# Kernel tuning notes

Measured on AMD Instinct MI355X. Metric: run time of the kernel, lower is better.

The kernel has to match this reference:

```python
import jax, jax.numpy as jnp
import numpy as np

ORDER, IN_DIM, OUT_DIM, SEQ_LEN = 4096, 8, 1, 4096


def setup_inputs() -> dict:
    key = jax.random.key(0)
    ks = jax.random.split(key, 7)
    # reset_parameter uses uniform(-0.7, 0.7); A/C/L rescaled ~1/sqrt(order) for
    # numerical stability of the 4096-step linear recurrence (same math, stable values).
    sA = 0.9 * (3.0 / ORDER) ** 0.5
    sC = 0.7 / ORDER ** 0.5
    weight_a = jax.random.uniform(ks[0], (ORDER, ORDER), minval=-sA, maxval=sA, dtype=jnp.float32)
    weight_b = jax.random.uniform(ks[1], (ORDER, IN_DIM), minval=-0.7, maxval=0.7, dtype=jnp.float32)
    weight_c = jax.random.uniform(ks[2], (OUT_DIM, ORDER), minval=-sC, maxval=sC, dtype=jnp.float32)
    weight_d = jax.random.uniform(ks[3], (OUT_DIM, IN_DIM), minval=-0.7, maxval=0.7, dtype=jnp.float32)
    weight_l = jax.random.uniform(ks[4], (ORDER, 1), minval=-sC, maxval=sC, dtype=jnp.float32)
    u = jax.random.normal(ks[5], (IN_DIM, SEQ_LEN), dtype=jnp.float32)
    y_obs = jax.random.normal(ks[6], (1, SEQ_LEN), dtype=jnp.float32)
    return {"u": u, "y_obs": y_obs, "weight_a": weight_a, "weight_b": weight_b,
            "weight_c": weight_c, "weight_d": weight_d, "weight_l": weight_l}


def reference(u, y_obs, weight_a, weight_b, weight_c, weight_d, weight_l):
    # Observer (Luenberger) state-space recursion, inp_dim > 1 branch:
    #   y_t  = C h_t + D u_t
    #   h_{t+1} = A h_t + B u_t + L * (y_obs_t - y_t)
    # output = tanh(concat(y_t)) * 3, shape [out_dim, seq_len]
    order = weight_a.shape[0]
    h0 = jnp.ones((order, 1), dtype=u.dtype)  # nn.init.constant_(hidden, 1)

    def step(h, inp):
        u_t, yobs_t = inp  # u_t: [in_dim, 1], yobs_t: scalar
        y_t = weight_c @ h + weight_d @ u_t          # [out_dim, 1]
        h_next = weight_a @ h + weight_b @ u_t + weight_l * (yobs_t - y_t)
        return h_next, y_t

    u_seq = u.T[:, :, None]          # [seq_len, in_dim, 1]
    _, ys = jax.lax.scan(step, h0, (u_seq, y_obs[0]))
    y_hat = ys[:, :, 0].T            # [out_dim, seq_len]
    return jnp.tanh(y_hat) * 3
```

## Files before the change

### kernel.cpp

```cpp
#include <hip/hip_runtime.h>
#include <math.h>


constexpr int NDIM  = 4096;
constexpr int NC    = 10;
constexpr int SLAB  = 16 * 4096;
constexpr int JT    = 56;
constexpr int VAPPS = 28;
constexpr int KC    = NDIM / 32;
constexpr int TILES = NDIM / 16;

typedef float    f32x4  __attribute__((ext_vector_type(4)));
typedef _Float16 h16x8  __attribute__((ext_vector_type(8)));
typedef _Float16 f16;

__global__ __launch_bounds__(256) void k_build_a(
        const float* __restrict__ A, const float* __restrict__ C,
        const float* __restrict__ L, h16x8* __restrict__ AhSw) {
    __shared__ float lds[64][65];
    const int R0 = (blockIdx.x & 63) * 64;
    const int C0 = (blockIdx.x >> 6) * 64;
    const int tid = threadIdx.x;
    #pragma unroll
    for (int it = 0; it < 16; ++it) {
        const int r = it * 4 + (tid >> 6);
        const int c = tid & 63;
        lds[r][c] = A[(size_t)(R0 + r) * NDIM + C0 + c]
                  - L[R0 + r] * C[C0 + c];
    }
    __syncthreads();
    #pragma unroll
    for (int half = 0; half < 2; ++half) {
        const int o = half * 256 + tid;
        const int r = o >> 3;
        const int g = o & 7;
        union { h16x8 v; f16 h[8]; } pk;
        #pragma unroll
        for (int j = 0; j < 8; ++j) pk.h[j] = (f16)lds[r][g * 8 + j];
        const int tile = (R0 >> 4) + (r >> 4);
        const int kc   = (C0 >> 5) + (g >> 2);
        const int lane = (r & 15) | ((g & 3) << 4);
        AhSw[((size_t)tile * KC + kc) * 64 + lane] = pk.v;
    }
}

__global__ __launch_bounds__(256) void k_build_w0(
        const float* __restrict__ Bm, const float* __restrict__ Dm,
        const float* __restrict__ L,
        float* __restrict__ Wf, f16* __restrict__ Wh) {
    int k = blockIdx.x * blockDim.x + threadIdx.x;
    float Lk = L[k];
    float col[16];
    #pragma unroll
    for (int c = 0; c < 8; ++c) col[c] = Bm[k * 8 + c] - Lk * Dm[c];
    col[8] = Lk; col[9] = 1.0f;
    #pragma unroll
    for (int c = 10; c < 16; ++c) col[c] = 0.0f;
    #pragma unroll
    for (int c = 0; c < 16; ++c) {
        Wf[c * NDIM + k] = col[c];
        Wh[c * NDIM + k] = (f16)col[c];
    }
}

__global__ __launch_bounds__(256) void k_stepVR(
        const h16x8* __restrict__ AhSw, const f16* __restrict__ WhIn,
        float* __restrict__ WfOut, f16* __restrict__ WhOut,
        const float* __restrict__ Cvec,
        const float* __restrict__ RpartIn, float* __restrict__ RpartOut,
        float* __restrict__ gfSlot, const int r) {
    const int tid = threadIdx.x;

    if (blockIdx.x < 128) {
        __shared__ f32x4 red[4][64];
        const int lane = tid & 63, wave = tid >> 6;
        const int mr   = lane & 15, q = lane >> 4;
        const int tp   = blockIdx.x;
        const int tile = tp * 2 + (wave >> 1);
        const int kh   = wave & 1;
        const int k0   = kh * 2048;
        const bool liveB = (mr < NC);
        const h16x8* a8 = AhSw + ((size_t)tile * KC + kh * 64) * 64 + lane;
        const h16x8* b8 = (const h16x8*)WhIn + (((size_t)mr * NDIM + k0) >> 3) + q;

        f32x4 acc0 = {0,0,0,0}, acc1 = {0,0,0,0};
        for (int it = 0; it < 8; ++it) {
            h16x8 ra[8], rb[8];
            #pragma unroll
            for (int s = 0; s < 8; ++s) rb[s] = (h16x8){0,0,0,0,0,0,0,0};
            #pragma unroll
            for (int s = 0; s < 8; ++s) {
                const int c = it * 8 + s;
                ra[s] = a8[(size_t)c * 64];
            }
            if (liveB) {
                #pragma unroll
                for (int s = 0; s < 8; ++s) {
                    const int c = it * 8 + s;
                    rb[s] = b8[c * 4];
                }
            }
            #pragma unroll
            for (int s = 0; s < 8; ++s) {
                if (s & 1) acc1 = __builtin_amdgcn_mfma_f32_16x16x32_f16(ra[s], rb[s], acc1, 0, 0, 0);
                else       acc0 = __builtin_amdgcn_mfma_f32_16x16x32_f16(ra[s], rb[s], acc0, 0, 0, 0);
            }
        }
        red[wave][lane] = acc0 + acc1;
        __syncthreads();
        if (tid < 128) {
            const int half = tid >> 6;
            const int l    = tid & 63;
            f32x4 v = red[half * 2][l] + red[half * 2 + 1][l];
            const int col = l & 15;
            if (col < NC) {
                const int row0 = (tp * 2 + half) * 16;
                const int rb0  = row0 + ((l >> 4) << 2);
                #pragma unroll
                for (int i = 0; i < 4; ++i) {
                    WfOut[col * NDIM + rb0 + i] = v[i];
                    WhOut[col * NDIM + rb0 + i] = (f16)v[i];
                }
            }
        }
    } else {
        __shared__ float rp[4096];
        __shared__ float g8[8][33];
        __shared__ float gs[32];
        const int t = blockIdx.x - 128;

        if (r == 0) {
            if (tid < 32) gs[tid] = Cvec[t * 32 + tid];
        } else {
            #pragma unroll
            for (int i = 0; i < 16; ++i) {
                const int idx = tid + i * 256;
                rp[idx] = RpartIn[(size_t)(idx >> 5) * NDIM + t * 32 + (idx & 31)];
            }
            __syncthreads();
            {
                const int c = tid & 31, g = tid >> 5;
                float s = 0.0f;
                #pragma unroll
                for (int j = 0; j < 16; ++j) s += rp[(g * 16 + j) * 32 + c];
                g8[g][c] = s;
            }
            __syncthreads();
            if (tid < 32) {
                float s = 0.0f;
                #pragma unroll
                for (int g = 0; g < 8; ++g) s += g8[g][tid];
                gs[tid] = s;
            }
        }
        __syncthreads();
        if (tid < 32) gfSlot[t * 32 + tid] = gs[tid];

        if (r < VAPPS - 1) {
            float gl[32];
            #pragma unroll
            for (int j = 0; j < 32; ++j) gl[j] = gs[j];
            #pragma unroll
            for (int cc = 0; cc < 2; ++cc) {
                const int ch = tid * 2 + cc;
                float acc[8] = {};
                #pragma unroll
                for (int tt = 0; tt < 2; ++tt) {
                    const h16x8* fr = AhSw + (size_t)(t * 2 + tt) * (KC * 64)
                                    + (size_t)ch * 16;
                    #pragma unroll
                    for (int mrr = 0; mrr < 16; ++mrr) {
                        union { h16x8 v; f16 h[8]; } ua;
                        ua.v = fr[mrr];
                        const float gm = gl[tt * 16 + mrr];
                        #pragma unroll
                        for (int j = 0; j < 8; ++j) acc[j] += gm * (float)ua.h[j];
                    }
                }
                float4* op = (float4*)(RpartOut + (size_t)t * NDIM + 8 * ch);
                op[0] = make_float4(acc[0], acc[1], acc[2], acc[3]);
                op[1] = make_float4(acc[4], acc[5], acc[6], acc[7]);
            }
        }
    }
}

__global__ __launch_bounds__(256) void k_fbatch(
        const float* __restrict__ Wall, const float* __restrict__ C,
        const float* __restrict__ gf, float* __restrict__ F) {
    const int m = blockIdx.x;
    const float* W;
    const float* vec;
    if (m <= VAPPS) { W = Wall + (size_t)m * SLAB;     vec = C; }
    else            { W = Wall + (size_t)VAPPS * SLAB; vec = gf + (size_t)(m - VAPPS) * NDIM; }
    const int tid = threadIdx.x, lane = tid & 63, wave = tid >> 6;
    float acc[NC] = {};
    for (int k = tid; k < NDIM; k += 256) {
        float ck = vec[k];
        #pragma unroll
        for (int c = 0; c < NC; ++c) acc[c] += ck * W[c * NDIM + k];
    }
    __shared__ float red[4][NC];
    #pragma unroll
    for (int c = 0; c < NC; ++c) {
        float s = acc[c];
        #pragma unroll
        for (int off = 32; off > 0; off >>= 1) s += __shfl_down(s, off);
        if (lane == 0) red[wave][c] = s;
    }
    __syncthreads();
    if (tid < NC) F[m * NC + tid] = red[0][tid] + red[1][tid] + red[2][tid] + red[3][tid];
}

__global__ __launch_bounds__(256) void k_conv(
        const float* __restrict__ F, const float* __restrict__ u,
        const float* __restrict__ yobs, const float* __restrict__ Dm,
        float* __restrict__ out) {
    __shared__ float Fl[JT * NC];
    __shared__ float zw[(JT + 256) * 9];
    const int tid = threadIdx.x;
    const int t0  = blockIdx.x * 256;
    for (int idx = tid; idx < JT * NC; idx += 256) Fl[idx] = F[idx];
    for (int idx = tid; idx < (JT + 256) * 9; idx += 256) {
        int k = idx / 9, c = idx - k * 9;
        int s = t0 - JT + k;
        float v = 0.0f;
        if (s >= 0 && s < NDIM) v = (c < 8) ? u[c * NDIM + s] : yobs[s];
        zw[idx] = v;
    }
    __syncthreads();
    const int t = t0 + tid;
    float y = (t < JT) ? Fl[t * NC + 9] : 0.0f;
    #pragma unroll
    for (int c = 0; c < 8; ++c) y += Dm[c] * u[c * NDIM + t];
    for (int j = 0; j < JT; ++j) {
        const float* fj = Fl + j * NC;
        const float* zz = zw + (tid + JT - 1 - j) * 9;
        float p = 0.0f;
        #pragma unroll
        for (int c = 0; c < 9; ++c) p += fj[c] * zz[c];
        y += p;
    }
    out[t] = 3.0f * tanhf(y);
}

extern "C" void kernel_launch(void* const* d_in, const int* in_sizes, int n_in,
                              void* d_out, int out_size, void* d_ws, size_t ws_size,
                              hipStream_t stream) {
    const float* u    = (const float*)d_in[0];
    const float* yobs = (const float*)d_in[1];
    const float* A    = (const float*)d_in[2];
    const float* Bm   = (const float*)d_in[3];
    const float* C    = (const float*)d_in[4];
    const float* Dm   = (const float*)d_in[5];
    const float* L    = (const float*)d_in[6];
    float* out = (float*)d_out;

    char* ws = (char*)d_ws;
    h16x8* AhSw  = (h16x8*)ws;
    float* Wf    = (float*)(ws + 33554432ull);
    f16*   Wh    = (f16*)(ws + 41156608ull);
    float* gf    = (float*)(ws + 44957696ull);
    float* Rpart = (float*)(ws + 45416448ull);
    float* F     = (float*)(ws + 49610752ull);

    constexpr size_t RPN = (size_t)128 * NDIM;

    k_build_a<<<dim3(64 * 64), dim3(256), 0, stream>>>(A, C, L, AhSw);
    k_build_w0<<<dim3(16), dim3(256), 0, stream>>>(Bm, Dm, L, Wf, Wh);

    for (int r = 0; r < VAPPS; ++r) {
        const size_t in   = (size_t)r * SLAB;
        const size_t out_ = (size_t)(r + 1) * SLAB;
        const float* rin  = Rpart + ((r + 1) & 1) * RPN;
        float*       rout = Rpart + (r & 1) * RPN;
        k_stepVR<<<dim3(256), dim3(256), 0, stream>>>(
            AhSw, Wh + in, Wf + out_, Wh + out_,
            C, rin, rout, gf + (size_t)r * NDIM, r);
    }

    k_fbatch<<<dim3(JT), dim3(256), 0, stream>>>(Wf, C, gf, F);
    k_conv<<<dim3(16), dim3(256), 0, stream>>>(F, u, yobs, Dm, out);
}
```

Measured before the change: 462.3 us.

## Fuse transposed A-vector product into MFMA step blocks, reusing loaded A fragments

The step kernel no longer splits its blocks into MFMA tiles and a separate set of blocks that reload A for the g·A product. Each of the 256 blocks now owns one 16-row tile, splits K across four waves, and computes the row-vector partials from the A fragments already held in registers, reducing them with cross-lane shuffles. The goal is to read A only once per step and balance work across all blocks. In exchange it adds shuffle-heavy ALU work inside the MFMA loop and doubles the size of the partial-sum buffer, which makes the reduction at the start of the next step larger.

```diff
diff --git a/kernel.cpp b/kernel.cpp
--- a/kernel.cpp
+++ b/kernel.cpp
@@ -63,123 +63,120 @@
     }
 }
 
-__global__ __launch_bounds__(256) void k_stepVR(
+__global__ __launch_bounds__(256) void k_step(
         const h16x8* __restrict__ AhSw, const f16* __restrict__ WhIn,
         float* __restrict__ WfOut, f16* __restrict__ WhOut,
         const float* __restrict__ Cvec,
         const float* __restrict__ RpartIn, float* __restrict__ RpartOut,
         float* __restrict__ gfSlot, const int r) {
-    const int tid = threadIdx.x;
-
-    if (blockIdx.x < 128) {
-        __shared__ f32x4 red[4][64];
-        const int lane = tid & 63, wave = tid >> 6;
-        const int mr   = lane & 15, q = lane >> 4;
-        const int tp   = blockIdx.x;
-        const int tile = tp * 2 + (wave >> 1);
-        const int kh   = wave & 1;
-        const int k0   = kh * 2048;
-        const bool liveB = (mr < NC);
-        const h16x8* a8 = AhSw + ((size_t)tile * KC + kh * 64) * 64 + lane;
-        const h16x8* b8 = (const h16x8*)WhIn + (((size_t)mr * NDIM + k0) >> 3) + q;
-
-        f32x4 acc0 = {0,0,0,0}, acc1 = {0,0,0,0};
-        for (int it = 0; it < 8; ++it) {
-            h16x8 ra[8], rb[8];
-            #pragma unroll
-            for (int s = 0; s < 8; ++s) rb[s] = (h16x8){0,0,0,0,0,0,0,0};
+    __shared__ f32x4 red[4][64];
+    __shared__ float rp[256][17];
+    __shared__ float g16[16][17];
+    __shared__ float gs[16];
+    const int tid  = threadIdx.x;
+    const int lane = tid & 63, wave = tid >> 6;
+    const int mr   = lane & 15, q = lane >> 4;
+    const int tile = blockIdx.x;
+    const int row0 = tile * 16;
+    const int k0   = wave * 1024;
+
+    if (r == 0) {
+        if (tid < 16) gs[tid] = Cvec[row0 + tid];
+    } else {
+        const float* src = RpartIn + (size_t)tid * NDIM + row0;
+        #pragma unroll
+        for (int j = 0; j < 16; j += 4) {
+            float4 v = *(const float4*)(src + j);
+            rp[tid][j] = v.x; rp[tid][j+1] = v.y;
+            rp[tid][j+2] = v.z; rp[tid][j+3] = v.w;
+        }
+        __syncthreads();
+        {
+            const int c = tid & 15, g = tid >> 4;
+            float s = 0.0f;
+            #pragma unroll
+            for (int j = 0; j < 16; ++j) s += rp[g * 16 + j][c];
+            g16[g][c] = s;
+        }
+        __syncthreads();
+        if (tid < 16) {
+            float s = 0.0f;
+            #pragma unroll
+            for (int g = 0; g < 16; ++g) s += g16[g][tid];
+            gs[tid] = s;
+        }
+    }
+    __syncthreads();
+    if (tid < 16) gfSlot[row0 + tid] = gs[tid];
+    const float gmr = gs[mr];
+    const bool doR = (r < VAPPS - 1);
+
+    const bool liveB = (mr < NC);
+    const h16x8* a8 = AhSw + ((size_t)tile * KC + wave * 32) * 64 + lane;
+    const h16x8* b8 = (const h16x8*)WhIn + (((size_t)mr * NDIM + k0) >> 3) + q;
+    float* rpo = RpartOut + (size_t)tile * NDIM;
+
+    f32x4 acc0 = {0,0,0,0}, acc1 = {0,0,0,0};
+    for (int it = 0; it < 4; ++it) {
+        h16x8 ra[8], rb[8];
+        #pragma unroll
+        for (int s = 0; s < 8; ++s) rb[s] = (h16x8){0,0,0,0,0,0,0,0};
+        #pragma unroll
+        for (int s = 0; s < 8; ++s) {
+            const int c = it * 8 + s;
+            ra[s] = a8[(size_t)c * 64];
+        }
+        if (liveB) {
             #pragma unroll
             for (int s = 0; s < 8; ++s) {
                 const int c = it * 8 + s;
-                ra[s] = a8[(size_t)c * 64];
+                rb[s] = b8[c * 4];
             }
-            if (liveB) {
+        }
+        #pragma unroll
+        for (int s = 0; s < 8; ++s) {
+            if (s & 1) acc1 = __builtin_amdgcn_mfma_f32_16x16x32_f16(ra[s], rb[s], acc1, 0, 0, 0);
+            else       acc0 = __builtin_amdgcn_mfma_f32_16x16x32_f16(ra[s], rb[s], acc0, 0, 0, 0);
+        }
+        if (doR) {
+            #pragma unroll
+            for (int s = 0; s < 8; ++s) {
+                union { h16x8 v; f16 h[8]; } ua;
+                ua.v = ra[s];
+                float p[8];
                 #pragma unroll
-                for (int s = 0; s < 8; ++s) {
-                    const int c = it * 8 + s;
-                    rb[s] = b8[c * 4];
+                for (int j = 0; j < 8; ++j) p[j] = gmr * (float)ua.h[j];
+                #pragma unroll
+                for (int off = 1; off < 16; off <<= 1) {
+                    #pragma unroll
+                    for (int j = 0; j < 8; ++j)
+                        p[j] += __shfl_xor(p[j], off, 16);
+                }
+                const float s01 = (mr & 1) ? p[1] : p[0];
+                const float s23 = (mr & 1) ? p[3] : p[2];
+                const float s45 = (mr & 1) ? p[5] : p[4];
+                const float s67 = (mr & 1) ? p[7] : p[6];
+                const float s03 = (mr & 2) ? s23 : s01;
+                const float s47 = (mr & 2) ? s67 : s45;
+                const float sel = (mr & 4) ? s47 : s03;
+                if (mr < 8) {
+                    const int kcG = wave * 32 + it * 8 + s;
+                    rpo[kcG * 32 + q * 8 + mr] = sel;
                 }
             }
-            #pragma unroll
-            for (int s = 0; s < 8; ++s) {
-                if (s & 1) acc1 = __builtin_amdgcn_mfma_f32_16x16x32_f16(ra[s], rb[s], acc1, 0, 0, 0);
-                else       acc0 = __builtin_amdgcn_mfma_f32_16x16x32_f16(ra[s], rb[s], acc0, 0, 0, 0);
-            }
-        }
-        red[wave][lane] = acc0 + acc1;
-        __syncthreads();
-        if (tid < 128) {
-            const int half = tid >> 6;
-            const int l    = tid & 63;
-            f32x4 v = red[half * 2][l] + red[half * 2 + 1][l];
-            const int col = l & 15;
-            if (col < NC) {
-                const int row0 = (tp * 2 + half) * 16;
-                const int rb0  = row0 + ((l >> 4) << 2);
-                #pragma unroll
-                for (int i = 0; i < 4; ++i) {
-                    WfOut[col * NDIM + rb0 + i] = v[i];
-                    WhOut[col * NDIM + rb0 + i] = (f16)v[i];
-                }
-            }
-        }
-    } else {
-        __shared__ float rp[4096];
-        __shared__ float g8[8][33];
-        __shared__ float gs[32];
-        const int t = blockIdx.x - 128;
-
-        if (r == 0) {
-            if (tid < 32) gs[tid] = Cvec[t * 32 + tid];
-        } else {
-            #pragma unroll
-            for (int i = 0; i < 16; ++i) {
-                const int idx = tid + i * 256;
-                rp[idx] = RpartIn[(size_t)(idx >> 5) * NDIM + t * 32 + (idx & 31)];
-            }
-            __syncthreads();
-            {
-                const int c = tid & 31, g = tid >> 5;
-                float s = 0.0f;
-                #pragma unroll
-                for (int j = 0; j < 16; ++j) s += rp[(g * 16 + j) * 32 + c];
-                g8[g][c] = s;
-            }
-            __syncthreads();
-            if (tid < 32) {
-                float s = 0.0f;
-                #pragma unroll
-                for (int g = 0; g < 8; ++g) s += g8[g][tid];
-                gs[tid] = s;
-            }
-        }
-        __syncthreads();
-        if (tid < 32) gfSlot[t * 32 + tid] = gs[tid];
-
-        if (r < VAPPS - 1) {
-            float gl[32];
-            #pragma unroll
-            for (int j = 0; j < 32; ++j) gl[j] = gs[j];
-            #pragma unroll
-            for (int cc = 0; cc < 2; ++cc) {
-                const int ch = tid * 2 + cc;
-                float acc[8] = {};
-                #pragma unroll
-                for (int tt = 0; tt < 2; ++tt) {
-                    const h16x8* fr = AhSw + (size_t)(t * 2 + tt) * (KC * 64)
-                                    + (size_t)ch * 16;
-                    #pragma unroll
-                    for (int mrr = 0; mrr < 16; ++mrr) {
-                        union { h16x8 v; f16 h[8]; } ua;
-                        ua.v = fr[mrr];
-                        const float gm = gl[tt * 16 + mrr];
-                        #pragma unroll
-                        for (int j = 0; j < 8; ++j) acc[j] += gm * (float)ua.h[j];
-                    }
-                }
-                float4* op = (float4*)(RpartOut + (size_t)t * NDIM + 8 * ch);
-                op[0] = make_float4(acc[0], acc[1], acc[2], acc[3]);
-                op[1] = make_float4(acc[4], acc[5], acc[6], acc[7]);
+        }
+    }
+    red[wave][lane] = acc0 + acc1;
+    __syncthreads();
+    if (tid < 64) {
+        f32x4 v = red[0][tid] + red[1][tid] + red[2][tid] + red[3][tid];
+        const int col = tid & 15;
+        if (col < NC) {
+            const int rb0 = row0 + ((tid >> 4) << 2);
+            #pragma unroll
+            for (int i = 0; i < 4; ++i) {
+                WfOut[col * NDIM + rb0 + i] = v[i];
+                WhOut[col * NDIM + rb0 + i] = (f16)v[i];
             }
         }
     }
@@ -262,9 +259,9 @@
     f16*   Wh    = (f16*)(ws + 41156608ull);
     float* gf    = (float*)(ws + 44957696ull);
     float* Rpart = (float*)(ws + 45416448ull);
-    float* F     = (float*)(ws + 49610752ull);
-
-    constexpr size_t RPN = (size_t)128 * NDIM;
+    float* F     = (float*)(ws + 53805056ull);
+
+    constexpr size_t RPN = (size_t)256 * NDIM;
 
     k_build_a<<<dim3(64 * 64), dim3(256), 0, stream>>>(A, C, L, AhSw);
     k_build_w0<<<dim3(16), dim3(256), 0, stream>>>(Bm, Dm, L, Wf, Wh);
@@ -274,7 +271,7 @@
         const size_t out_ = (size_t)(r + 1) * SLAB;
         const float* rin  = Rpart + ((r + 1) & 1) * RPN;
         float*       rout = Rpart + (r & 1) * RPN;
-        k_stepVR<<<dim3(256), dim3(256), 0, stream>>>(
+        k_step<<<dim3(256), dim3(256), 0, stream>>>(
             AhSw, Wh + in, Wf + out_, Wh + out_,
             C, rin, rout, gf + (size_t)r * NDIM, r);
     }
```

New measurement: 696.2 us. 1.51x slower.

## Fuse per-step kernel launches into one persistent cooperative kernel with grid barriers

Applied to the files above, without the earlier changes.

Replaces the 28 separate k_stepVR launches with a single cooperative persistent kernel. Blocks step through all iterations and synchronise through atomic counters in global memory, using cache-bypassing loads and stores. MFMA blocks now stage the full f16 B slab into LDS each step, replacing the per-wave global reads. This is meant to remove launch overhead and inter-kernel gaps. In exchange it adds spin-barrier latency, requires all 256 blocks to be co-resident, and loads each slab redundantly into every block's LDS.

```diff
diff --git a/kernel.cpp b/kernel.cpp
--- a/kernel.cpp
+++ b/kernel.cpp
@@ -9,6 +9,7 @@
 constexpr int VAPPS = 28;
 constexpr int KC    = NDIM / 32;
 constexpr int TILES = NDIM / 16;
+constexpr size_t RPN = (size_t)128 * NDIM;
 
 typedef float    f32x4  __attribute__((ext_vector_type(4)));
 typedef _Float16 h16x8  __attribute__((ext_vector_type(8)));
@@ -47,8 +48,10 @@
 __global__ __launch_bounds__(256) void k_build_w0(
         const float* __restrict__ Bm, const float* __restrict__ Dm,
         const float* __restrict__ L,
-        float* __restrict__ Wf, f16* __restrict__ Wh) {
+        float* __restrict__ Wf, f16* __restrict__ Wh,
+        unsigned int* __restrict__ flags) {
     int k = blockIdx.x * blockDim.x + threadIdx.x;
+    if (k < 64) flags[k] = 0u;
     float Lk = L[k];
     float col[16];
     #pragma unroll
@@ -63,124 +66,201 @@
     }
 }
 
-__global__ __launch_bounds__(256) void k_stepVR(
-        const h16x8* __restrict__ AhSw, const f16* __restrict__ WhIn,
-        float* __restrict__ WfOut, f16* __restrict__ WhOut,
-        const float* __restrict__ Cvec,
-        const float* __restrict__ RpartIn, float* __restrict__ RpartOut,
-        float* __restrict__ gfSlot, const int r) {
-    const int tid = threadIdx.x;
-
-    if (blockIdx.x < 128) {
-        __shared__ f32x4 red[4][64];
-        const int lane = tid & 63, wave = tid >> 6;
-        const int mr   = lane & 15, q = lane >> 4;
-        const int tp   = blockIdx.x;
+__global__ __launch_bounds__(256, 1) void k_persist(
+        const h16x8* __restrict__ AhSw, f16* __restrict__ WhB,
+        float* __restrict__ Wf, const float* __restrict__ Cvec,
+        float* __restrict__ gf, float* __restrict__ Rpart,
+        unsigned int* __restrict__ flags) {
+    __shared__ f16   Bst[10][4104];
+    __shared__ f32x4 red[4][64];
+    __shared__ float rp[128][36];
+    __shared__ float g8v[8][33];
+    __shared__ float gs[32];
+    const int tid  = threadIdx.x;
+    const int bid  = blockIdx.x;
+    const int lane = tid & 63, wave = tid >> 6;
+    const int mr   = lane & 15, q = lane >> 4;
+
+    if (bid < 128) {
+        const int tp = bid;
         const int tile = tp * 2 + (wave >> 1);
         const int kh   = wave & 1;
-        const int k0   = kh * 2048;
         const bool liveB = (mr < NC);
-        const h16x8* a8 = AhSw + ((size_t)tile * KC + kh * 64) * 64 + lane;
-        const h16x8* b8 = (const h16x8*)WhIn + (((size_t)mr * NDIM + k0) >> 3) + q;
-
-        f32x4 acc0 = {0,0,0,0}, acc1 = {0,0,0,0};
-        for (int it = 0; it < 8; ++it) {
-            h16x8 ra[8], rb[8];
-            #pragma unroll
-            for (int s = 0; s < 8; ++s) rb[s] = (h16x8){0,0,0,0,0,0,0,0};
-            #pragma unroll
-            for (int s = 0; s < 8; ++s) {
-                const int c = it * 8 + s;
-                ra[s] = a8[(size_t)c * 64];
-            }
-            if (liveB) {
+        const h16x8* a8 = AhSw + ((size_t)tile * KC + (size_t)kh * 64) * 64 + lane;
+        const f16* bl = &Bst[0][0] + (size_t)mr * 4104 + kh * 2048 + q * 8;
+
+        for (int r = 0; r < VAPPS; ++r) {
+            {
+                const f16* p = WhB + (size_t)r * SLAB + (size_t)tid * 160;
+                f32x4 b0,b1,b2,b3,b4,b5,b6,b7,b8,b9,b10,b11,b12,b13,b14,b15,b16,b17,b18,b19;
+                asm volatile(
+                    "global_load_dwordx4 %0, %20, off sc0 sc1\n\t"
+                    "global_load_dwordx4 %1, %20, off offset:16 sc0 sc1\n\t"
+                    "global_load_dwordx4 %2, %20, off offset:32 sc0 sc1\n\t"
+                    "global_load_dwordx4 %3, %20, off offset:48 sc0 sc1\n\t"
+                    "global_load_dwordx4 %4, %20, off offset:64 sc0 sc1\n\t"
+                    "global_load_dwordx4 %5, %20, off offset:80 sc0 sc1\n\t"
+                    "global_load_dwordx4 %6, %20, off offset:96 sc0 sc1\n\t"
+                    "global_load_dwordx4 %7, %20, off offset:112 sc0 sc1\n\t"
+                    "global_load_dwordx4 %8, %20, off offset:128 sc0 sc1\n\t"
+                    "global_load_dwordx4 %9, %20, off offset:144 sc0 sc1\n\t"
+                    "global_load_dwordx4 %10, %20, off offset:160 sc0 sc1\n\t"
+                    "global_load_dwordx4 %11, %20, off offset:176 sc0 sc1\n\t"
+                    "global_load_dwordx4 %12, %20, off offset:192 sc0 sc1\n\t"
+                    "global_load_dwordx4 %13, %20, off offset:208 sc0 sc1\n\t"
+                    "global_load_dwordx4 %14, %20, off offset:224 sc0 sc1\n\t"
+                    "global_load_dwordx4 %15, %20, off offset:240 sc0 sc1\n\t"
+                    "global_load_dwordx4 %16, %20, off offset:256 sc0 sc1\n\t"
+                    "global_load_dwordx4 %17, %20, off offset:272 sc0 sc1\n\t"
+                    "global_load_dwordx4 %18, %20, off offset:288 sc0 sc1\n\t"
+                    "global_load_dwordx4 %19, %20, off offset:304 sc0 sc1\n\t"
+                    "s_waitcnt vmcnt(0)"
+                    : "=&v"(b0),"=&v"(b1),"=&v"(b2),"=&v"(b3),"=&v"(b4),
+                      "=&v"(b5),"=&v"(b6),"=&v"(b7),"=&v"(b8),"=&v"(b9),
+                      "=&v"(b10),"=&v"(b11),"=&v"(b12),"=&v"(b13),"=&v"(b14),
+                      "=&v"(b15),"=&v"(b16),"=&v"(b17),"=&v"(b18),"=&v"(b19)
+                    : "v"(p) : "memory");
+                f32x4 bb[20] = {b0,b1,b2,b3,b4,b5,b6,b7,b8,b9,b10,b11,
+                                b12,b13,b14,b15,b16,b17,b18,b19};
+                const int u0 = tid * 20;
+                #pragma unroll
+                for (int i = 0; i < 20; ++i) {
+                    const int u = u0 + i;
+                    union { f32x4 f; h16x8 h; } cv; cv.f = bb[i];
+                    *(h16x8*)&Bst[u >> 9][(u & 511) * 8] = cv.h;
+                }
+            }
+            __syncthreads();
+
+            f32x4 acc0 = {0,0,0,0}, acc1 = {0,0,0,0};
+            for (int it = 0; it < 8; ++it) {
+                h16x8 ra[8], rb[8];
+                #pragma unroll
+                for (int s = 0; s < 8; ++s) rb[s] = (h16x8){0,0,0,0,0,0,0,0};
+                #pragma unroll
+                for (int s = 0; s < 8; ++s) ra[s] = a8[(size_t)(it * 8 + s) * 64];
+                if (liveB) {
+                    #pragma unroll
+                    for (int s = 0; s < 8; ++s)
+                        rb[s] = *(const h16x8*)(bl + (it * 8 + s) * 32);
+                }
                 #pragma unroll
                 for (int s = 0; s < 8; ++s) {
-                    const int c = it * 8 + s;
-                    rb[s] = b8[c * 4];
-                }
-            }
-            #pragma unroll
-            for (int s = 0; s < 8; ++s) {
-                if (s & 1) acc1 = __builtin_amdgcn_mfma_f32_16x16x32_f16(ra[s], rb[s], acc1, 0, 0, 0);
-                else       acc0 = __builtin_amdgcn_mfma_f32_16x16x32_f16(ra[s], rb[s], acc0, 0, 0, 0);
-            }
-        }
-        red[wave][lane] = acc0 + acc1;
-        __syncthreads();
-        if (tid < 128) {
-            const int half = tid >> 6;
-            const int l    = tid & 63;
-            f32x4 v = red[half * 2][l] + red[half * 2 + 1][l];
-            const int col = l & 15;
-            if (col < NC) {
-                const int row0 = (tp * 2 + half) * 16;
-                const int rb0  = row0 + ((l >> 4) << 2);
-                #pragma unroll
-                for (int i = 0; i < 4; ++i) {
-                    WfOut[col * NDIM + rb0 + i] = v[i];
-                    WhOut[col * NDIM + rb0 + i] = (f16)v[i];
-                }
-            }
+                    if (s & 1) acc1 = __builtin_amdgcn_mfma_f32_16x16x32_f16(ra[s], rb[s], acc1, 0, 0, 0);
+                    else       acc0 = __builtin_amdgcn_mfma_f32_16x16x32_f16(ra[s], rb[s], acc0, 0, 0, 0);
+                }
+            }
+            red[wave][lane] = acc0 + acc1;
+            __syncthreads();
+            if (tid < 128) {
+                const int half = tid >> 6, l = tid & 63;
+                f32x4 v = red[half * 2][l] + red[half * 2 + 1][l];
+                const int col = l & 15;
+                if (col < NC) {
+                    const int rb0 = (tp * 2 + half) * 16 + ((l >> 4) << 2);
+                    float* wf = Wf + (size_t)(r + 1) * SLAB + (size_t)col * NDIM + rb0;
+                    #pragma unroll
+                    for (int i = 0; i < 4; ++i)
+                        __builtin_nontemporal_store(v[i], wf + i);
+                    union { f16 h[4]; int2 u2; } pk;
+                    #pragma unroll
+                    for (int i = 0; i < 4; ++i) pk.h[i] = (f16)v[i];
+                    f16* wh = WhB + (size_t)(r + 1) * SLAB + (size_t)col * NDIM + rb0;
+                    asm volatile("global_store_dwordx2 %0, %1, off sc0 sc1"
+                                 :: "v"(wh), "v"(pk.u2) : "memory");
+                }
+            }
+            asm volatile("s_waitcnt vmcnt(0)" ::: "memory");
+            __syncthreads();
+            if (tid == 0) {
+                __hip_atomic_fetch_add(&flags[r], 1u, __ATOMIC_RELAXED, __HIP_MEMORY_SCOPE_AGENT);
+                while (__hip_atomic_load(&flags[r], __ATOMIC_RELAXED, __HIP_MEMORY_SCOPE_AGENT) < 256u)
+                    __builtin_amdgcn_s_sleep(2);
+            }
+            __syncthreads();
         }
     } else {
-        __shared__ float rp[4096];
-        __shared__ float g8[8][33];
-        __shared__ float gs[32];
-        const int t = blockIdx.x - 128;
-
-        if (r == 0) {
-            if (tid < 32) gs[tid] = Cvec[t * 32 + tid];
-        } else {
-            #pragma unroll
-            for (int i = 0; i < 16; ++i) {
-                const int idx = tid + i * 256;
-                rp[idx] = RpartIn[(size_t)(idx >> 5) * NDIM + t * 32 + (idx & 31)];
-            }
-            __syncthreads();
-            {
-                const int c = tid & 31, g = tid >> 5;
-                float s = 0.0f;
-                #pragma unroll
-                for (int j = 0; j < 16; ++j) s += rp[(g * 16 + j) * 32 + c];
-                g8[g][c] = s;
-            }
-            __syncthreads();
-            if (tid < 32) {
-                float s = 0.0f;
-                #pragma unroll
-                for (int g = 0; g < 8; ++g) s += g8[g][tid];
-                gs[tid] = s;
-            }
-        }
-        __syncthreads();
-        if (tid < 32) gfSlot[t * 32 + tid] = gs[tid];
-
-        if (r < VAPPS - 1) {
-            float gl[32];
-            #pragma unroll
-            for (int j = 0; j < 32; ++j) gl[j] = gs[j];
-            #pragma unroll
-            for (int cc = 0; cc < 2; ++cc) {
-                const int ch = tid * 2 + cc;
-                float acc[8] = {};
-                #pragma unroll
-                for (int tt = 0; tt < 2; ++tt) {
-                    const h16x8* fr = AhSw + (size_t)(t * 2 + tt) * (KC * 64)
-                                    + (size_t)ch * 16;
-                    #pragma unroll
-                    for (int mrr = 0; mrr < 16; ++mrr) {
-                        union { h16x8 v; f16 h[8]; } ua;
-                        ua.v = fr[mrr];
-                        const float gm = gl[tt * 16 + mrr];
+        const int t = bid - 128;
+        for (int r = 0; r < VAPPS; ++r) {
+            if (r == 0) {
+                if (tid < 32) gs[tid] = Cvec[t * 32 + tid];
+                __syncthreads();
+            } else {
+                const float* RpIn = Rpart + (size_t)((r + 1) & 1) * RPN;
+                const int p = tid >> 1, c0 = (tid & 1) * 16;
+                const float* q4 = RpIn + (size_t)p * NDIM + t * 32 + c0;
+                f32x4 v0, v1, v2, v3;
+                asm volatile(
+                    "global_load_dwordx4 %0, %4, off sc0 sc1\n\t"
+                    "global_load_dwordx4 %1, %4, off offset:16 sc0 sc1\n\t"
+                    "global_load_dwordx4 %2, %4, off offset:32 sc0 sc1\n\t"
+                    "global_load_dwordx4 %3, %4, off offset:48 sc0 sc1\n\t"
+                    "s_waitcnt vmcnt(0)"
+                    : "=&v"(v0), "=&v"(v1), "=&v"(v2), "=&v"(v3)
+                    : "v"(q4) : "memory");
+                *(f32x4*)&rp[p][c0]      = v0;
+                *(f32x4*)&rp[p][c0 + 4]  = v1;
+                *(f32x4*)&rp[p][c0 + 8]  = v2;
+                *(f32x4*)&rp[p][c0 + 12] = v3;
+                __syncthreads();
+                {
+                    const int c = tid & 31, g = tid >> 5;
+                    float s = 0.0f;
+                    #pragma unroll
+                    for (int j = 0; j < 16; ++j) s += rp[g * 16 + j][c];
+                    g8v[g][c] = s;
+                }
+                __syncthreads();
+                if (tid < 32) {
+                    float s = 0.0f;
+                    #pragma unroll
+                    for (int g = 0; g < 8; ++g) s += g8v[g][tid];
+                    gs[tid] = s;
+                }
+                __syncthreads();
+            }
+            if (tid < 32)
+                __builtin_nontemporal_store(gs[tid], gf + (size_t)r * NDIM + t * 32 + tid);
+
+            if (r < VAPPS - 1) {
+                float gl[32];
+                #pragma unroll
+                for (int j = 0; j < 32; ++j) gl[j] = gs[j];
+                float* RpOut = Rpart + (size_t)(r & 1) * RPN + (size_t)t * NDIM;
+                #pragma unroll
+                for (int cc = 0; cc < 2; ++cc) {
+                    const int ch = tid * 2 + cc;
+                    float acc[8] = {};
+                    #pragma unroll
+                    for (int tt = 0; tt < 2; ++tt) {
+                        const h16x8* fr = AhSw + (size_t)(t * 2 + tt) * (KC * 64)
+                                        + (size_t)ch * 16;
                         #pragma unroll
-                        for (int j = 0; j < 8; ++j) acc[j] += gm * (float)ua.h[j];
+                        for (int mrr = 0; mrr < 16; ++mrr) {
+                            union { h16x8 v; f16 h[8]; } ua;
+                            ua.v = fr[mrr];
+                            const float gm = gl[tt * 16 + mrr];
+                            #pragma unroll
+                            for (int j = 0; j < 8; ++j) acc[j] += gm * (float)ua.h[j];
+                        }
                     }
-                }
-                float4* op = (float4*)(RpartOut + (size_t)t * NDIM + 8 * ch);
-                op[0] = make_float4(acc[0], acc[1], acc[2], acc[3]);
-                op[1] = make_float4(acc[4], acc[5], acc[6], acc[7]);
-            }
+                    f32x4 o0 = {acc[0], acc[1], acc[2], acc[3]};
+                    f32x4 o1 = {acc[4], acc[5], acc[6], acc[7]};
+                    float* op = RpOut + 8 * ch;
+                    asm volatile(
+                        "global_store_dwordx4 %0, %2, off sc0 sc1\n\t"
+                        "global_store_dwordx4 %1, %3, off sc0 sc1"
+                        :: "v"(op), "v"(op + 4), "v"(o0), "v"(o1) : "memory");
+                }
+            }
+            asm volatile("s_waitcnt vmcnt(0)" ::: "memory");
+            __syncthreads();
+            if (tid == 0) {
+                __hip_atomic_fetch_add(&flags[r], 1u, __ATOMIC_RELAXED, __HIP_MEMORY_SCOPE_AGENT);
+                while (__hip_atomic_load(&flags[r], __ATOMIC_RELAXED, __HIP_MEMORY_SCOPE_AGENT) < 256u)
+                    __builtin_amdgcn_s_sleep(2);
+            }
+            __syncthreads();
         }
     }
 }
@@ -257,26 +337,22 @@
     float* out = (float*)d_out;
 
     char* ws = (char*)d_ws;
-    h16x8* AhSw  = (h16x8*)ws;
-    float* Wf    = (float*)(ws + 33554432ull);
-    f16*   Wh    = (f16*)(ws + 41156608ull);
-    float* gf    = (float*)(ws + 44957696ull);
-    float* Rpart = (float*)(ws + 45416448ull);
-    float* F     = (float*)(ws + 49610752ull);
-
-    constexpr size_t RPN = (size_t)128 * NDIM;
+    h16x8*        AhSw  = (h16x8*)ws;
+    float*        Wf    = (float*)(ws + 33554432ull);
+    f16*          Wh    = (f16*)(ws + 41156608ull);
+    float*        gf    = (float*)(ws + 44957696ull);
+    float*        Rpart = (float*)(ws + 45416448ull);
+    float*        F     = (float*)(ws + 49610752ull);
+    unsigned int* flags = (unsigned int*)(ws + 49614848ull);
 
     k_build_a<<<dim3(64 * 64), dim3(256), 0, stream>>>(A, C, L, AhSw);
-    k_build_w0<<<dim3(16), dim3(256), 0, stream>>>(Bm, Dm, L, Wf, Wh);
-
-    for (int r = 0; r < VAPPS; ++r) {
-        const size_t in   = (size_t)r * SLAB;
-        const size_t out_ = (size_t)(r + 1) * SLAB;
-        const float* rin  = Rpart + ((r + 1) & 1) * RPN;
-        float*       rout = Rpart + (r & 1) * RPN;
-        k_stepVR<<<dim3(256), dim3(256), 0, stream>>>(
-            AhSw, Wh + in, Wf + out_, Wh + out_,
-            C, rin, rout, gf + (size_t)r * NDIM, r);
+    k_build_w0<<<dim3(16), dim3(256), 0, stream>>>(Bm, Dm, L, Wf, Wh, flags);
+
+    {
+        void* args[] = { (void*)&AhSw, (void*)&Wh, (void*)&Wf, (void*)&C,
+                         (void*)&gf, (void*)&Rpart, (void*)&flags };
+        (void)hipLaunchCooperativeKernel((const void*)k_persist, dim3(256), dim3(256),
+                                         args, 0u, stream);
     }
 
     k_fbatch<<<dim3(JT), dim3(256), 0, stream>>>(Wf, C, gf, F);
```

New measurement: 773.4 us. 1.67x slower.

## Quantize A-LC to 12-bit per-row scaled ints split into 8+4 bit planes

Applied to the files above, without the earlier changes.

Adds a per-row absmax pass and a quantization kernel that stores the fp16 A−LC matrix as a signed 8-bit high plane plus a 4-bit nibble plane with per-row scales. The repeated step kernels read these 12-bit values, dequantize them to fp16 in registers for MFMA and for the VR reduction, and apply the row scale on output. The goal is to cut the bytes of A read in each of the 28 step launches. In exchange it adds an extra setup kernel, ALU work for unpacking, and a 12-bit precision loss on A.

```diff
diff --git a/kernel.cpp b/kernel.cpp
--- a/kernel.cpp
+++ b/kernel.cpp
@@ -16,7 +16,8 @@
 
 __global__ __launch_bounds__(256) void k_build_a(
         const float* __restrict__ A, const float* __restrict__ C,
-        const float* __restrict__ L, h16x8* __restrict__ AhSw) {
+        const float* __restrict__ L, h16x8* __restrict__ AhSwH,
+        unsigned int* __restrict__ rowmaxU) {
     __shared__ float lds[64][65];
     const int R0 = (blockIdx.x & 63) * 64;
     const int C0 = (blockIdx.x >> 6) * 64;
@@ -29,6 +30,12 @@
                   - L[R0 + r] * C[C0 + c];
     }
     __syncthreads();
+    if (tid < 64) {
+        float mx = 0.0f;
+        #pragma unroll 8
+        for (int c = 0; c < 64; ++c) mx = fmaxf(mx, fabsf(lds[tid][c]));
+        atomicMax(&rowmaxU[R0 + tid], __float_as_uint(mx));
+    }
     #pragma unroll
     for (int half = 0; half < 2; ++half) {
         const int o = half * 256 + tid;
@@ -40,15 +47,47 @@
         const int tile = (R0 >> 4) + (r >> 4);
         const int kc   = (C0 >> 5) + (g >> 2);
         const int lane = (r & 15) | ((g & 3) << 4);
-        AhSw[((size_t)tile * KC + kc) * 64 + lane] = pk.v;
-    }
+        AhSwH[((size_t)tile * KC + kc) * 64 + lane] = pk.v;
+    }
+}
+
+__global__ __launch_bounds__(256) void k_quant_a(
+        const h16x8* __restrict__ AhSwH, const unsigned int* __restrict__ rowmaxU,
+        long* __restrict__ A8, unsigned int* __restrict__ A4,
+        float* __restrict__ sA) {
+    const size_t idx = (size_t)blockIdx.x * blockDim.x + threadIdx.x;
+    const int lane = (int)(idx & 63);
+    const int mr   = lane & 15;
+    const int tile = (int)(idx >> 13);
+    const int row  = tile * 16 + mr;
+    const float rm  = __uint_as_float(rowmaxU[row]);
+    const float inv = rm > 0.0f ? 2039.0f / rm : 0.0f;
+    union { h16x8 v; f16 h[8]; } uh;
+    uh.v = AhSwH[idx];
+    union { long l; signed char c[8]; } uo;
+    unsigned int lo = 0u;
+    #pragma unroll
+    for (int j = 0; j < 8; ++j) {
+        int qv = (int)rintf((float)uh.h[j] * inv);
+        qv = qv > 2039 ? 2039 : (qv < -2039 ? -2039 : qv);
+        const int hi  = (qv + 8) >> 4;
+        const int nib = qv - (hi << 4) + 8;
+        uo.c[j] = (signed char)hi;
+        lo |= (unsigned int)nib << (4 * j);
+    }
+    A8[idx] = uo.l;
+    A4[idx] = lo;
+    if (((idx >> 6) & (KC - 1)) == 0 && (lane >> 4) == 0)
+        sA[row] = rm / 2039.0f;
 }
 
 __global__ __launch_bounds__(256) void k_build_w0(
         const float* __restrict__ Bm, const float* __restrict__ Dm,
         const float* __restrict__ L,
-        float* __restrict__ Wf, f16* __restrict__ Wh) {
+        float* __restrict__ Wf, f16* __restrict__ Wh,
+        unsigned int* __restrict__ rowmaxU) {
     int k = blockIdx.x * blockDim.x + threadIdx.x;
+    rowmaxU[k] = 0u;
     float Lk = L[k];
     float col[16];
     #pragma unroll
@@ -64,7 +103,8 @@
 }
 
 __global__ __launch_bounds__(256) void k_stepVR(
-        const h16x8* __restrict__ AhSw, const f16* __restrict__ WhIn,
+        const long* __restrict__ A8, const unsigned int* __restrict__ A4,
+        const float* __restrict__ sA, const f16* __restrict__ WhIn,
         float* __restrict__ WfOut, f16* __restrict__ WhOut,
         const float* __restrict__ Cvec,
         const float* __restrict__ RpartIn, float* __restrict__ RpartOut,
@@ -80,46 +120,55 @@
         const int kh   = wave & 1;
         const int k0   = kh * 2048;
         const bool liveB = (mr < NC);
-        const h16x8* a8 = AhSw + ((size_t)tile * KC + kh * 64) * 64 + lane;
+        const size_t abase = ((size_t)tile * KC + (size_t)kh * 64) * 64 + lane;
+        const long*         a8 = A8 + abase;
+        const unsigned int* a4 = A4 + abase;
         const h16x8* b8 = (const h16x8*)WhIn + (((size_t)mr * NDIM + k0) >> 3) + q;
 
         f32x4 acc0 = {0,0,0,0}, acc1 = {0,0,0,0};
         for (int it = 0; it < 8; ++it) {
-            h16x8 ra[8], rb[8];
+            long ral[8]; unsigned int rln[8]; h16x8 rb[8];
             #pragma unroll
             for (int s = 0; s < 8; ++s) rb[s] = (h16x8){0,0,0,0,0,0,0,0};
             #pragma unroll
             for (int s = 0; s < 8; ++s) {
-                const int c = it * 8 + s;
-                ra[s] = a8[(size_t)c * 64];
+                ral[s] = a8[(size_t)(it * 8 + s) * 64];
+                rln[s] = a4[(size_t)(it * 8 + s) * 64];
             }
             if (liveB) {
                 #pragma unroll
-                for (int s = 0; s < 8; ++s) {
-                    const int c = it * 8 + s;
-                    rb[s] = b8[c * 4];
+                for (int s = 0; s < 8; ++s)
+                    rb[s] = b8[(it * 8 + s) * 4];
+            }
+            #pragma unroll
+            for (int s = 0; s < 8; ++s) {
+                union { long l; signed char c[8]; } ua;
+                ua.l = ral[s];
+                const unsigned int lo = rln[s];
+                h16x8 af;
+                #pragma unroll
+                for (int j = 0; j < 8; ++j) {
+                    const int qv = ((int)ua.c[j] << 4)
+                                 + (int)((lo >> (4 * j)) & 15u) - 8;
+                    af[j] = (f16)(float)qv;
                 }
-            }
-            #pragma unroll
-            for (int s = 0; s < 8; ++s) {
-                if (s & 1) acc1 = __builtin_amdgcn_mfma_f32_16x16x32_f16(ra[s], rb[s], acc1, 0, 0, 0);
-                else       acc0 = __builtin_amdgcn_mfma_f32_16x16x32_f16(ra[s], rb[s], acc0, 0, 0, 0);
+                if (s & 1) acc1 = __builtin_amdgcn_mfma_f32_16x16x32_f16(af, rb[s], acc1, 0, 0, 0);
+                else       acc0 = __builtin_amdgcn_mfma_f32_16x16x32_f16(af, rb[s], acc0, 0, 0, 0);
             }
         }
         red[wave][lane] = acc0 + acc1;
         __syncthreads();
         if (tid < 128) {
-            const int half = tid >> 6;
-            const int l    = tid & 63;
+            const int half = tid >> 6, l = tid & 63;
             f32x4 v = red[half * 2][l] + red[half * 2 + 1][l];
             const int col = l & 15;
             if (col < NC) {
-                const int row0 = (tp * 2 + half) * 16;
-                const int rb0  = row0 + ((l >> 4) << 2);
+                const int rb0 = (tp * 2 + half) * 16 + ((l >> 4) << 2);
                 #pragma unroll
                 for (int i = 0; i < 4; ++i) {
-                    WfOut[col * NDIM + rb0 + i] = v[i];
-                    WhOut[col * NDIM + rb0 + i] = (f16)v[i];
+                    const float vv = v[i] * sA[rb0 + i];
+                    WfOut[col * NDIM + rb0 + i] = vv;
+                    WhOut[col * NDIM + rb0 + i] = (f16)vv;
                 }
             }
         }
@@ -159,22 +208,29 @@
         if (r < VAPPS - 1) {
             float gl[32];
             #pragma unroll
-            for (int j = 0; j < 32; ++j) gl[j] = gs[j];
+            for (int j = 0; j < 32; ++j) gl[j] = gs[j] * sA[t * 32 + j];
             #pragma unroll
             for (int cc = 0; cc < 2; ++cc) {
                 const int ch = tid * 2 + cc;
                 float acc[8] = {};
                 #pragma unroll
                 for (int tt = 0; tt < 2; ++tt) {
-                    const h16x8* fr = AhSw + (size_t)(t * 2 + tt) * (KC * 64)
+                    const size_t fb = (size_t)(t * 2 + tt) * (KC * 64)
                                     + (size_t)ch * 16;
+                    const long*         fr8 = A8 + fb;
+                    const unsigned int* fr4 = A4 + fb;
                     #pragma unroll
                     for (int mrr = 0; mrr < 16; ++mrr) {
-                        union { h16x8 v; f16 h[8]; } ua;
-                        ua.v = fr[mrr];
+                        union { long l; signed char c[8]; } ua;
+                        ua.l = fr8[mrr];
+                        const unsigned int lo = fr4[mrr];
                         const float gm = gl[tt * 16 + mrr];
                         #pragma unroll
-                        for (int j = 0; j < 8; ++j) acc[j] += gm * (float)ua.h[j];
+                        for (int j = 0; j < 8; ++j) {
+                            const int qv = ((int)ua.c[j] << 4)
+                                         + (int)((lo >> (4 * j)) & 15u) - 8;
+                            acc[j] += gm * (float)qv;
+                        }
                     }
                 }
                 float4* op = (float4*)(RpartOut + (size_t)t * NDIM + 8 * ch);
@@ -257,17 +313,22 @@
     float* out = (float*)d_out;
 
     char* ws = (char*)d_ws;
-    h16x8* AhSw  = (h16x8*)ws;
-    float* Wf    = (float*)(ws + 33554432ull);
-    f16*   Wh    = (f16*)(ws + 41156608ull);
-    float* gf    = (float*)(ws + 44957696ull);
-    float* Rpart = (float*)(ws + 45416448ull);
-    float* F     = (float*)(ws + 49610752ull);
+    h16x8*        AhSwH   = (h16x8*)ws;
+    long*         A8      = (long*)(ws + 33554432ull);
+    unsigned int* A4      = (unsigned int*)(ws + 50331648ull);
+    float*        Wf      = (float*)(ws + 58720256ull);
+    f16*          Wh      = (f16*)(ws + 66322432ull);
+    float*        gf      = (float*)(ws + 70123520ull);
+    float*        Rpart   = (float*)(ws + 70582272ull);
+    float*        F       = (float*)(ws + 74776576ull);
+    float*        sA      = (float*)(ws + 74780672ull);
+    unsigned int* rowmaxU = (unsigned int*)(ws + 74797056ull);
 
     constexpr size_t RPN = (size_t)128 * NDIM;
 
-    k_build_a<<<dim3(64 * 64), dim3(256), 0, stream>>>(A, C, L, AhSw);
-    k_build_w0<<<dim3(16), dim3(256), 0, stream>>>(Bm, Dm, L, Wf, Wh);
+    k_build_w0<<<dim3(16), dim3(256), 0, stream>>>(Bm, Dm, L, Wf, Wh, rowmaxU);
+    k_build_a<<<dim3(64 * 64), dim3(256), 0, stream>>>(A, C, L, AhSwH, rowmaxU);
+    k_quant_a<<<dim3(TILES * KC * 64 / 256), dim3(256), 0, stream>>>(AhSwH, rowmaxU, A8, A4, sA);
 
     for (int r = 0; r < VAPPS; ++r) {
         const size_t in   = (size_t)r * SLAB;
@@ -275,7 +336,7 @@
         const float* rin  = Rpart + ((r + 1) & 1) * RPN;
         float*       rout = Rpart + (r & 1) * RPN;
         k_stepVR<<<dim3(256), dim3(256), 0, stream>>>(
-            AhSw, Wh + in, Wf + out_, Wh + out_,
+            A8, A4, sA, Wh + in, Wf + out_, Wh + out_,
             C, rin, rout, gf + (size_t)r * NDIM, r);
     }
 
```

Result: slower. 535.3 us (+15.8%).
